# Performance work log

Measured on AMD Instinct MI355X. Metric: run time of the kernel, lower is better.

Reference implementation:

```python
import jax, jax.numpy as jnp
import numpy as np

B, C, H, W = 4, 3, 512, 960
K2 = 16  # 4x4 adaptive filter, DAIN-style


def setup_inputs() -> dict:
    key = jax.random.key(0)
    k1, k2, k3 = jax.random.split(key, 3)
    teninput = jax.random.normal(k1, (B, C, H, W), dtype=jnp.float32)
    tenflow = jax.random.normal(k2, (B, 2, H, W), dtype=jnp.float32)
    tenfilter = jax.random.uniform(k3, (B, K2, H, W), dtype=jnp.float32)
    return {"teninput": teninput, "tenflow": tenflow, "tenfilter": tenfilter}


def reference(teninput, tenflow, tenfilter):
    # DAIN FilterInterpolation forward:
    # out[b,c,y,x] = valid * sum_{dj,di < K} filter[b, dj*K+di, y, x]
    #               * bilinear(input, y2_T + dj + beta, x2_L + di + alpha)
    # with per-corner clamped gathers; out-of-bounds flow targets give 0.
    b, c, h, w = teninput.shape
    k2 = tenfilter.shape[1]
    K = int(np.sqrt(k2))

    dt = teninput.dtype
    xs = jnp.arange(w, dtype=dt)[None, None, :]
    ys = jnp.arange(h, dtype=dt)[None, :, None]
    fx, fy = tenflow[:, 0], tenflow[:, 1]          # [B,H,W]
    x2 = xs + fx
    y2 = ys + fy
    valid = ((x2 >= 0) & (x2 <= w - 1) & (y2 >= 0) & (y2 <= h - 1)
             & (jnp.abs(fx) < w / 2) & (jnp.abs(fy) < h / 2))

    ix = jnp.floor(x2).astype(jnp.int32)
    iy = jnp.floor(y2).astype(jnp.int32)
    alpha = (x2 - ix)[:, None]                     # [B,1,H,W]
    beta = (y2 - iy)[:, None]
    ixL0 = ix + 1 - K // 2                         # window left edge
    iyT0 = iy + 1 - K // 2                         # window top edge

    inp_flat = teninput.reshape(b, c, h * w)

    def gather(yi, xi):  # yi, xi: [B,H,W] int -> [B,C,H,W]
        idx = (yi * w + xi).reshape(b, 1, h * w)
        return jnp.take_along_axis(inp_flat, idx, axis=2).reshape(b, c, h, w)

    wTL = (1 - alpha) * (1 - beta)
    wTR = alpha * (1 - beta)
    wBL = (1 - alpha) * beta
    wBR = alpha * beta

    out = jnp.zeros_like(teninput)
    for dj in range(K):
        yT = jnp.clip(iyT0 + dj, 0, h - 1)
        yB = jnp.clip(iyT0 + dj + 1, 0, h - 1)
        for di in range(K):
            xL = jnp.clip(ixL0 + di, 0, w - 1)
            xR = jnp.clip(ixL0 + di + 1, 0, w - 1)
            val = (wTL * gather(yT, xL) + wTR * gather(yT, xR)
                   + wBL * gather(yB, xL) + wBR * gather(yB, xR))
            out = out + val * tenfilter[:, dj * K + di][:, None]

    return out * valid[:, None].astype(dt)
```

## Files before the change

### kernel.cpp

```cpp
#include <hip/hip_runtime.h>

#define BB 4
#define CC 3
#define HH 512
#define WW 960
#define HW (HH * WW)
#define NPIX (BB * HW)

__global__ __launch_bounds__(256)
void filter_interp_kernel(const float* __restrict__ inp,
                          const float* __restrict__ flow,
                          const float* __restrict__ filt,
                          float* __restrict__ out) {
    int tid = blockIdx.x * blockDim.x + threadIdx.x;
    if (tid >= NPIX) return;

    int b   = tid / HW;
    int rem = tid - b * HW;
    int y   = rem / WW;
    int x   = rem - y * WW;

    const float fx = flow[(b * 2 + 0) * HW + rem];
    const float fy = flow[(b * 2 + 1) * HW + rem];
    const float x2 = (float)x + fx;
    const float y2 = (float)y + fy;

    bool valid = (x2 >= 0.0f) && (x2 <= (float)(WW - 1)) &&
                 (y2 >= 0.0f) && (y2 <= (float)(HH - 1)) &&
                 (fabsf(fx) < (float)WW * 0.5f) &&
                 (fabsf(fy) < (float)HH * 0.5f);

    const int outbase = b * CC * HW + rem;
    if (!valid) {
        out[outbase]          = 0.0f;
        out[outbase + HW]     = 0.0f;
        out[outbase + 2 * HW] = 0.0f;
        return;
    }

    const int ix = (int)floorf(x2);
    const int iy = (int)floorf(y2);
    const float alpha = x2 - (float)ix;
    const float beta  = y2 - (float)iy;

    const float wTL = (1.0f - alpha) * (1.0f - beta);
    const float wTR = alpha * (1.0f - beta);
    const float wBL = (1.0f - alpha) * beta;
    const float wBR = alpha * beta;

    const int ixL0 = ix - 1;
    const int iyT0 = iy - 1;

    int R[5];
#pragma unroll
    for (int j = 0; j < 5; ++j) R[j] = min(max(iyT0 + j, 0), HH - 1);

    float Wm[5][5];
#pragma unroll
    for (int j = 0; j < 5; ++j)
#pragma unroll
        for (int i = 0; i < 5; ++i) Wm[j][i] = 0.0f;

    const float* fptr = filt + (size_t)b * 16 * HW + rem;
#pragma unroll
    for (int dj = 0; dj < 4; ++dj) {
#pragma unroll
        for (int di = 0; di < 4; ++di) {
            const float f = fptr[(size_t)(dj * 4 + di) * HW];
            Wm[dj][di]         += f * wTL;
            Wm[dj][di + 1]     += f * wTR;
            Wm[dj + 1][di]     += f * wBL;
            Wm[dj + 1][di + 1] += f * wBR;
        }
    }

    const float* ibase = inp + (size_t)b * CC * HW;
    float acc[3] = {0.0f, 0.0f, 0.0f};

    if (ixL0 >= 0 && ixL0 + 4 <= WW - 1) {
        const int a0 = ixL0 & ~3;
        const int o  = ixL0 - a0;

        const bool s2 = (o & 2) != 0;
        const bool s1 = (o & 1) != 0;
        float We[5][8];
#pragma unroll
        for (int j = 0; j < 5; ++j) {
            float t[8];
#pragma unroll
            for (int i = 0; i < 8; ++i) t[i] = (i < 5) ? Wm[j][i] : 0.0f;
            float u[8];
#pragma unroll
            for (int i = 0; i < 8; ++i)
                u[i] = s2 ? ((i >= 2) ? t[i - 2] : 0.0f) : t[i];
#pragma unroll
            for (int i = 0; i < 8; ++i)
                We[j][i] = s1 ? ((i >= 1) ? u[i - 1] : 0.0f) : u[i];
        }

#pragma unroll
        for (int j = 0; j < 5; ++j) {
            const size_t rowoff = (size_t)R[j] * WW + a0;
#pragma unroll
            for (int c = 0; c < CC; ++c) {
                const float* rp = ibase + (size_t)c * HW + rowoff;
                const float4 p0 = *(const float4*)(rp);
                const float4 p1 = *(const float4*)(rp + 4);
                float a = acc[c];
                a += p0.x * We[j][0];
                a += p0.y * We[j][1];
                a += p0.z * We[j][2];
                a += p0.w * We[j][3];
                a += p1.x * We[j][4];
                a += p1.y * We[j][5];
                a += p1.z * We[j][6];
                a += p1.w * We[j][7];
                acc[c] = a;
            }
        }
    } else {
        int S[5];
#pragma unroll
        for (int i = 0; i < 5; ++i) S[i] = min(max(ixL0 + i, 0), WW - 1);
#pragma unroll
        for (int c = 0; c < CC; ++c) {
            const float* ic = ibase + (size_t)c * HW;
            float a = 0.0f;
#pragma unroll
            for (int j = 0; j < 5; ++j) {
                const float* row = ic + (size_t)R[j] * WW;
#pragma unroll
                for (int i = 0; i < 5; ++i) a += row[S[i]] * Wm[j][i];
            }
            acc[c] = a;
        }
    }

    out[outbase]          = acc[0];
    out[outbase + HW]     = acc[1];
    out[outbase + 2 * HW] = acc[2];
}

extern "C" void kernel_launch(void* const* d_in, const int* in_sizes, int n_in,
                              void* d_out, int out_size, void* d_ws, size_t ws_size,
                              hipStream_t stream) {
    const float* teninput  = (const float*)d_in[0];
    const float* tenflow   = (const float*)d_in[1];
    const float* tenfilter = (const float*)d_in[2];
    float* out = (float*)d_out;

    const int threads = 256;
    const int blocks  = (NPIX + threads - 1) / threads;
    filter_interp_kernel<<<blocks, threads, 0, stream>>>(teninput, tenflow, tenfilter, out);
}
```

Before: 236.9 us.

## Stage input tile with halo in LDS for filter interpolation gathers

Each block now handles a 64x4 pixel tile and first cooperatively loads a 24x92 halo region of all three input channels into shared memory. Per-pixel 5x5 gathers are then served from shared memory when the flow target stays within the halo, with a global-memory fallback otherwise. This replaces scattered global gathers with shared reads, at the cost of a block-wide sync, redundant halo loading and higher LDS usage per block.

```diff
diff --git a/kernel.cpp b/kernel.cpp
--- a/kernel.cpp
+++ b/kernel.cpp
@@ -7,135 +7,171 @@
 #define HW (HH * WW)
 #define NPIX (BB * HW)
 
+#define TLX 64
+#define TLY 4
+#define NTX (WW / TLX)
+#define NTY (HH / TLY)
+#define NR 24
+#define RPAD 9
+#define NCOL 92
+#define CPAD 12
+
 __global__ __launch_bounds__(256)
-void filter_interp_kernel(const float* __restrict__ inp,
-                          const float* __restrict__ flow,
-                          const float* __restrict__ filt,
-                          float* __restrict__ out) {
-    int tid = blockIdx.x * blockDim.x + threadIdx.x;
-    if (tid >= NPIX) return;
+void filter_interp_tiled(const float* __restrict__ inp,
+                         const float* __restrict__ flow,
+                         const float* __restrict__ filt,
+                         float* __restrict__ out) {
+    const int lx = threadIdx.x & 63;
+    const int ly = threadIdx.x >> 6;
+    int blk = blockIdx.x;
+    const int tx = blk % NTX; blk /= NTX;
+    const int ty = blk % NTY;
+    const int b  = blk / NTY;
+    const int x0 = tx * TLX;
+    const int y0 = ty * TLY;
+    const int x  = x0 + lx;
+    const int y  = y0 + ly;
+    const int rem = y * WW + x;
 
-    int b   = tid / HW;
-    int rem = tid - b * HW;
-    int y   = rem / WW;
-    int x   = rem - y * WW;
+    __shared__ __align__(16) float sm[CC * NR * NCOL];
+
+    const float* ib = inp + (size_t)b * CC * HW;
+    const int c0 = x0 - CPAD;
+    const int r0 = y0 - RPAD;
+    for (int idx = threadIdx.x; idx < CC * NR * (NCOL / 4); idx += 256) {
+        const int ch = idx / (NR * (NCOL / 4));
+        const int rm = idx - ch * NR * (NCOL / 4);
+        const int r  = rm / (NCOL / 4);
+        const int m  = rm - r * (NCOL / 4);
+        const int gr = min(max(r0 + r, 0), HH - 1);
+        const int gcb = c0 + 4 * m;
+        const float* rowp = ib + (size_t)ch * HW + (size_t)gr * WW;
+        float4 v;
+        if (gcb >= 0 && gcb + 3 < WW) {
+            v = *(const float4*)(rowp + gcb);
+        } else {
+            v.x = rowp[min(max(gcb,     0), WW - 1)];
+            v.y = rowp[min(max(gcb + 1, 0), WW - 1)];
+            v.z = rowp[min(max(gcb + 2, 0), WW - 1)];
+            v.w = rowp[min(max(gcb + 3, 0), WW - 1)];
+        }
+        *(float4*)(&sm[(ch * NR + r) * NCOL + 4 * m]) = v;
+    }
+    __syncthreads();
 
     const float fx = flow[(b * 2 + 0) * HW + rem];
     const float fy = flow[(b * 2 + 1) * HW + rem];
     const float x2 = (float)x + fx;
     const float y2 = (float)y + fy;
 
-    bool valid = (x2 >= 0.0f) && (x2 <= (float)(WW - 1)) &&
-                 (y2 >= 0.0f) && (y2 <= (float)(HH - 1)) &&
-                 (fabsf(fx) < (float)WW * 0.5f) &&
-                 (fabsf(fy) < (float)HH * 0.5f);
+    const bool valid = (x2 >= 0.0f) && (x2 <= (float)(WW - 1)) &&
+                       (y2 >= 0.0f) && (y2 <= (float)(HH - 1)) &&
+                       (fabsf(fx) < (float)WW * 0.5f) &&
+                       (fabsf(fy) < (float)HH * 0.5f);
 
-    const int outbase = b * CC * HW + rem;
-    if (!valid) {
-        out[outbase]          = 0.0f;
-        out[outbase + HW]     = 0.0f;
-        out[outbase + 2 * HW] = 0.0f;
-        return;
-    }
+    float acc[3] = {0.0f, 0.0f, 0.0f};
 
-    const int ix = (int)floorf(x2);
-    const int iy = (int)floorf(y2);
-    const float alpha = x2 - (float)ix;
-    const float beta  = y2 - (float)iy;
+    if (valid) {
+        const int ix = (int)floorf(x2);
+        const int iy = (int)floorf(y2);
+        const float alpha = x2 - (float)ix;
+        const float beta  = y2 - (float)iy;
 
-    const float wTL = (1.0f - alpha) * (1.0f - beta);
-    const float wTR = alpha * (1.0f - beta);
-    const float wBL = (1.0f - alpha) * beta;
-    const float wBR = alpha * beta;
+        const float wTL = (1.0f - alpha) * (1.0f - beta);
+        const float wTR = alpha * (1.0f - beta);
+        const float wBL = (1.0f - alpha) * beta;
+        const float wBR = alpha * beta;
 
-    const int ixL0 = ix - 1;
-    const int iyT0 = iy - 1;
+        float Wm[5][5];
+#pragma unroll
+        for (int j = 0; j < 5; ++j)
+#pragma unroll
+            for (int i = 0; i < 5; ++i) Wm[j][i] = 0.0f;
 
-    int R[5];
+        const float* fptr = filt + (size_t)b * 16 * HW + rem;
 #pragma unroll
-    for (int j = 0; j < 5; ++j) R[j] = min(max(iyT0 + j, 0), HH - 1);
+        for (int dj = 0; dj < 4; ++dj) {
+#pragma unroll
+            for (int di = 0; di < 4; ++di) {
+                const float f = fptr[(size_t)(dj * 4 + di) * HW];
+                Wm[dj][di]         += f * wTL;
+                Wm[dj][di + 1]     += f * wTR;
+                Wm[dj + 1][di]     += f * wBL;
+                Wm[dj + 1][di + 1] += f * wBR;
+            }
+        }
 
-    float Wm[5][5];
+        const int ixL0 = ix - 1;
+        const int iyT0 = iy - 1;
+        const int k0 = iyT0 - r0;
+        const int d  = ixL0 - c0;
+        const int a0 = d & ~3;
+        const int o  = d & 3;
+
+        const bool fast = (k0 >= 0) && (k0 <= NR - 5) &&
+                          (d >= 0) && (a0 + 8 <= NCOL);
+
+        if (fast) {
+            const bool s2 = (o & 2) != 0;
+            const bool s1 = (o & 1) != 0;
+            float We[5][8];
 #pragma unroll
-    for (int j = 0; j < 5; ++j)
+            for (int j = 0; j < 5; ++j) {
+                float t[8];
 #pragma unroll
-        for (int i = 0; i < 5; ++i) Wm[j][i] = 0.0f;
+                for (int i = 0; i < 8; ++i) t[i] = (i < 5) ? Wm[j][i] : 0.0f;
+                float u[8];
+#pragma unroll
+                for (int i = 0; i < 8; ++i)
+                    u[i] = s2 ? ((i >= 2) ? t[i - 2] : 0.0f) : t[i];
+#pragma unroll
+                for (int i = 0; i < 8; ++i)
+                    We[j][i] = s1 ? ((i >= 1) ? u[i - 1] : 0.0f) : u[i];
+            }
 
-    const float* fptr = filt + (size_t)b * 16 * HW + rem;
 #pragma unroll
-    for (int dj = 0; dj < 4; ++dj) {
+            for (int j = 0; j < 5; ++j) {
+                const int rowbase = (k0 + j) * NCOL + a0;
 #pragma unroll
-        for (int di = 0; di < 4; ++di) {
-            const float f = fptr[(size_t)(dj * 4 + di) * HW];
-            Wm[dj][di]         += f * wTL;
-            Wm[dj][di + 1]     += f * wTR;
-            Wm[dj + 1][di]     += f * wBL;
-            Wm[dj + 1][di + 1] += f * wBR;
+                for (int c = 0; c < CC; ++c) {
+                    const float* sp = &sm[c * (NR * NCOL) + rowbase];
+                    const float4 p0 = *(const float4*)(sp);
+                    const float4 p1 = *(const float4*)(sp + 4);
+                    float a = acc[c];
+                    a += p0.x * We[j][0];
+                    a += p0.y * We[j][1];
+                    a += p0.z * We[j][2];
+                    a += p0.w * We[j][3];
+                    a += p1.x * We[j][4];
+                    a += p1.y * We[j][5];
+                    a += p1.z * We[j][6];
+                    a += p1.w * We[j][7];
+                    acc[c] = a;
+                }
+            }
+        } else {
+            int S[5], R[5];
+#pragma unroll
+            for (int i = 0; i < 5; ++i) {
+                S[i] = min(max(ixL0 + i, 0), WW - 1);
+                R[i] = min(max(iyT0 + i, 0), HH - 1);
+            }
+#pragma unroll
+            for (int c = 0; c < CC; ++c) {
+                const float* ic = ib + (size_t)c * HW;
+                float a = 0.0f;
+#pragma unroll
+                for (int j = 0; j < 5; ++j) {
+                    const float* row = ic + (size_t)R[j] * WW;
+#pragma unroll
+                    for (int i = 0; i < 5; ++i) a += row[S[i]] * Wm[j][i];
+                }
+                acc[c] = a;
+            }
         }
     }
 
-    const float* ibase = inp + (size_t)b * CC * HW;
-    float acc[3] = {0.0f, 0.0f, 0.0f};
-
-    if (ixL0 >= 0 && ixL0 + 4 <= WW - 1) {
-        const int a0 = ixL0 & ~3;
-        const int o  = ixL0 - a0;
-
-        const bool s2 = (o & 2) != 0;
-        const bool s1 = (o & 1) != 0;
-        float We[5][8];
-#pragma unroll
-        for (int j = 0; j < 5; ++j) {
-            float t[8];
-#pragma unroll
-            for (int i = 0; i < 8; ++i) t[i] = (i < 5) ? Wm[j][i] : 0.0f;
-            float u[8];
-#pragma unroll
-            for (int i = 0; i < 8; ++i)
-                u[i] = s2 ? ((i >= 2) ? t[i - 2] : 0.0f) : t[i];
-#pragma unroll
-            for (int i = 0; i < 8; ++i)
-                We[j][i] = s1 ? ((i >= 1) ? u[i - 1] : 0.0f) : u[i];
-        }
-
-#pragma unroll
-        for (int j = 0; j < 5; ++j) {
-            const size_t rowoff = (size_t)R[j] * WW + a0;
-#pragma unroll
-            for (int c = 0; c < CC; ++c) {
-                const float* rp = ibase + (size_t)c * HW + rowoff;
-                const float4 p0 = *(const float4*)(rp);
-                const float4 p1 = *(const float4*)(rp + 4);
-                float a = acc[c];
-                a += p0.x * We[j][0];
-                a += p0.y * We[j][1];
-                a += p0.z * We[j][2];
-                a += p0.w * We[j][3];
-                a += p1.x * We[j][4];
-                a += p1.y * We[j][5];
-                a += p1.z * We[j][6];
-                a += p1.w * We[j][7];
-                acc[c] = a;
-            }
-        }
-    } else {
-        int S[5];
-#pragma unroll
-        for (int i = 0; i < 5; ++i) S[i] = min(max(ixL0 + i, 0), WW - 1);
-#pragma unroll
-        for (int c = 0; c < CC; ++c) {
-            const float* ic = ibase + (size_t)c * HW;
-            float a = 0.0f;
-#pragma unroll
-            for (int j = 0; j < 5; ++j) {
-                const float* row = ic + (size_t)R[j] * WW;
-#pragma unroll
-                for (int i = 0; i < 5; ++i) a += row[S[i]] * Wm[j][i];
-            }
-            acc[c] = a;
-        }
-    }
-
+    const int outbase = b * CC * HW + rem;
     out[outbase]          = acc[0];
     out[outbase + HW]     = acc[1];
     out[outbase + 2 * HW] = acc[2];
@@ -149,7 +185,6 @@
     const float* tenfilter = (const float*)d_in[2];
     float* out = (float*)d_out;
 
-    const int threads = 256;
-    const int blocks  = (NPIX + threads - 1) / threads;
-    filter_interp_kernel<<<blocks, threads, 0, stream>>>(teninput, tenflow, tenfilter, out);
+    const int blocks = NTX * NTY * BB;
+    filter_interp_tiled<<<blocks, 256, 0, stream>>>(teninput, tenflow, tenfilter, out);
 }
```

New measurement: 255.9 us. 8.0% more time.

## Process four pixels per thread with vectorized flow, filter and output access

Applied to the files above, without the earlier changes.

Each thread now handles four horizontally adjacent pixels and loads flow, the 16 filter planes, and output stores as float4 vectors instead of scalar accesses. The gather work per pixel is unchanged and runs in a serial loop over the four pixels. This aims to cut memory instruction count and improve streaming efficiency on the dominant filter traffic. In exchange it raises register pressure (16 f4 filter values held live), lowers the thread count, and reduces latency hiding for the random gathers. Launch bounds now request 2 blocks per CU.

```diff
diff --git a/kernel.cpp b/kernel.cpp
--- a/kernel.cpp
+++ b/kernel.cpp
@@ -5,140 +5,156 @@
 #define HH 512
 #define WW 960
 #define HW (HH * WW)
-#define NPIX (BB * HW)
+#define NQ (BB * HW / 4)
 
-__global__ __launch_bounds__(256)
-void filter_interp_kernel(const float* __restrict__ inp,
-                          const float* __restrict__ flow,
-                          const float* __restrict__ filt,
-                          float* __restrict__ out) {
-    int tid = blockIdx.x * blockDim.x + threadIdx.x;
-    if (tid >= NPIX) return;
+typedef float f4 __attribute__((ext_vector_type(4)));
 
-    int b   = tid / HW;
-    int rem = tid - b * HW;
-    int y   = rem / WW;
-    int x   = rem - y * WW;
+__global__ __launch_bounds__(256, 2)
+void filter_interp_quad(const float* __restrict__ inp,
+                        const float* __restrict__ flow,
+                        const float* __restrict__ filt,
+                        float* __restrict__ out) {
+    const int t = blockIdx.x * 256 + threadIdx.x;
+    const int qpb = HW / 4;
+    const int b   = t / qpb;
+    const int q   = t - b * qpb;
+    const int y   = q / (WW / 4);
+    const int x0  = (q - y * (WW / 4)) * 4;
+    const int rem = y * WW + x0;
 
-    const float fx = flow[(b * 2 + 0) * HW + rem];
-    const float fy = flow[(b * 2 + 1) * HW + rem];
-    const float x2 = (float)x + fx;
-    const float y2 = (float)y + fy;
+    const f4 fx4 = *(const f4*)(flow + (size_t)(b * 2 + 0) * HW + rem);
+    const f4 fy4 = *(const f4*)(flow + (size_t)(b * 2 + 1) * HW + rem);
 
-    bool valid = (x2 >= 0.0f) && (x2 <= (float)(WW - 1)) &&
-                 (y2 >= 0.0f) && (y2 <= (float)(HH - 1)) &&
-                 (fabsf(fx) < (float)WW * 0.5f) &&
-                 (fabsf(fy) < (float)HH * 0.5f);
+    f4 ft[16];
+    const float* fb = filt + (size_t)b * 16 * HW + rem;
+#pragma unroll
+    for (int k = 0; k < 16; ++k) ft[k] = *(const f4*)(fb + (size_t)k * HW);
 
-    const int outbase = b * CC * HW + rem;
-    if (!valid) {
-        out[outbase]          = 0.0f;
-        out[outbase + HW]     = 0.0f;
-        out[outbase + 2 * HW] = 0.0f;
-        return;
+    const float* ib = inp + (size_t)b * CC * HW;
+
+    f4 accv[CC];
+#pragma unroll
+    for (int c = 0; c < CC; ++c) accv[c] = (f4){0.f, 0.f, 0.f, 0.f};
+
+#pragma unroll
+    for (int p = 0; p < 4; ++p) {
+        const float fx = fx4[p];
+        const float fy = fy4[p];
+        const int   xp = x0 + p;
+        const float x2 = (float)xp + fx;
+        const float y2 = (float)y + fy;
+
+        const bool valid = (x2 >= 0.0f) && (x2 <= (float)(WW - 1)) &&
+                           (y2 >= 0.0f) && (y2 <= (float)(HH - 1)) &&
+                           (fabsf(fx) < (float)WW * 0.5f) &&
+                           (fabsf(fy) < (float)HH * 0.5f);
+        if (!valid) continue;
+
+        const int ix = (int)floorf(x2);
+        const int iy = (int)floorf(y2);
+        const float alpha = x2 - (float)ix;
+        const float beta  = y2 - (float)iy;
+
+        const float wTL = (1.0f - alpha) * (1.0f - beta);
+        const float wTR = alpha * (1.0f - beta);
+        const float wBL = (1.0f - alpha) * beta;
+        const float wBR = alpha * beta;
+
+        float Wm[5][5];
+#pragma unroll
+        for (int j = 0; j < 5; ++j)
+#pragma unroll
+            for (int i = 0; i < 5; ++i) Wm[j][i] = 0.0f;
+#pragma unroll
+        for (int dj = 0; dj < 4; ++dj) {
+#pragma unroll
+            for (int di = 0; di < 4; ++di) {
+                const float f = ft[dj * 4 + di][p];
+                Wm[dj][di]         += f * wTL;
+                Wm[dj][di + 1]     += f * wTR;
+                Wm[dj + 1][di]     += f * wBL;
+                Wm[dj + 1][di + 1] += f * wBR;
+            }
+        }
+
+        const int ixL0 = ix - 1;
+        const int iyT0 = iy - 1;
+        int R[5];
+#pragma unroll
+        for (int j = 0; j < 5; ++j) R[j] = min(max(iyT0 + j, 0), HH - 1);
+
+        float a0c = 0.f, a1c = 0.f, a2c = 0.f;
+
+        if (ixL0 >= 0 && ixL0 + 4 <= WW - 1) {
+            const int a0 = ixL0 & ~3;
+            const int o  = ixL0 - a0;
+            const bool s2 = (o & 2) != 0;
+            const bool s1 = (o & 1) != 0;
+            float We[5][8];
+#pragma unroll
+            for (int j = 0; j < 5; ++j) {
+                float tt[8];
+#pragma unroll
+                for (int i = 0; i < 8; ++i) tt[i] = (i < 5) ? Wm[j][i] : 0.0f;
+                float u[8];
+#pragma unroll
+                for (int i = 0; i < 8; ++i)
+                    u[i] = s2 ? ((i >= 2) ? tt[i - 2] : 0.0f) : tt[i];
+#pragma unroll
+                for (int i = 0; i < 8; ++i)
+                    We[j][i] = s1 ? ((i >= 1) ? u[i - 1] : 0.0f) : u[i];
+            }
+
+#pragma unroll
+            for (int j = 0; j < 5; ++j) {
+                const size_t rowoff = (size_t)R[j] * WW + a0;
+                const float* r0p = ib + rowoff;
+                const float* r1p = r0p + HW;
+                const float* r2p = r1p + HW;
+                const f4 q00 = *(const f4*)(r0p);
+                const f4 q01 = *(const f4*)(r0p + 4);
+                const f4 q10 = *(const f4*)(r1p);
+                const f4 q11 = *(const f4*)(r1p + 4);
+                const f4 q20 = *(const f4*)(r2p);
+                const f4 q21 = *(const f4*)(r2p + 4);
+#pragma unroll
+                for (int i = 0; i < 4; ++i) {
+                    a0c += q00[i] * We[j][i];
+                    a0c += q01[i] * We[j][i + 4];
+                    a1c += q10[i] * We[j][i];
+                    a1c += q11[i] * We[j][i + 4];
+                    a2c += q20[i] * We[j][i];
+                    a2c += q21[i] * We[j][i + 4];
+                }
+            }
+        } else {
+            int S[5];
+#pragma unroll
+            for (int i = 0; i < 5; ++i) S[i] = min(max(ixL0 + i, 0), WW - 1);
+            float* accp[3] = {&a0c, &a1c, &a2c};
+#pragma unroll
+            for (int c = 0; c < CC; ++c) {
+                const float* ic = ib + (size_t)c * HW;
+                float a = 0.0f;
+#pragma unroll
+                for (int j = 0; j < 5; ++j) {
+                    const float* row = ic + (size_t)R[j] * WW;
+#pragma unroll
+                    for (int i = 0; i < 5; ++i) a += row[S[i]] * Wm[j][i];
+                }
+                *accp[c] = a;
+            }
+        }
+
+        accv[0][p] = a0c;
+        accv[1][p] = a1c;
+        accv[2][p] = a2c;
     }
 
-    const int ix = (int)floorf(x2);
-    const int iy = (int)floorf(y2);
-    const float alpha = x2 - (float)ix;
-    const float beta  = y2 - (float)iy;
-
-    const float wTL = (1.0f - alpha) * (1.0f - beta);
-    const float wTR = alpha * (1.0f - beta);
-    const float wBL = (1.0f - alpha) * beta;
-    const float wBR = alpha * beta;
-
-    const int ixL0 = ix - 1;
-    const int iyT0 = iy - 1;
-
-    int R[5];
-#pragma unroll
-    for (int j = 0; j < 5; ++j) R[j] = min(max(iyT0 + j, 0), HH - 1);
-
-    float Wm[5][5];
-#pragma unroll
-    for (int j = 0; j < 5; ++j)
-#pragma unroll
-        for (int i = 0; i < 5; ++i) Wm[j][i] = 0.0f;
-
-    const float* fptr = filt + (size_t)b * 16 * HW + rem;
-#pragma unroll
-    for (int dj = 0; dj < 4; ++dj) {
-#pragma unroll
-        for (int di = 0; di < 4; ++di) {
-            const float f = fptr[(size_t)(dj * 4 + di) * HW];
-            Wm[dj][di]         += f * wTL;
-            Wm[dj][di + 1]     += f * wTR;
-            Wm[dj + 1][di]     += f * wBL;
-            Wm[dj + 1][di + 1] += f * wBR;
-        }
-    }
-
-    const float* ibase = inp + (size_t)b * CC * HW;
-    float acc[3] = {0.0f, 0.0f, 0.0f};
-
-    if (ixL0 >= 0 && ixL0 + 4 <= WW - 1) {
-        const int a0 = ixL0 & ~3;
-        const int o  = ixL0 - a0;
-
-        const bool s2 = (o & 2) != 0;
-        const bool s1 = (o & 1) != 0;
-        float We[5][8];
-#pragma unroll
-        for (int j = 0; j < 5; ++j) {
-            float t[8];
-#pragma unroll
-            for (int i = 0; i < 8; ++i) t[i] = (i < 5) ? Wm[j][i] : 0.0f;
-            float u[8];
-#pragma unroll
-            for (int i = 0; i < 8; ++i)
-                u[i] = s2 ? ((i >= 2) ? t[i - 2] : 0.0f) : t[i];
-#pragma unroll
-            for (int i = 0; i < 8; ++i)
-                We[j][i] = s1 ? ((i >= 1) ? u[i - 1] : 0.0f) : u[i];
-        }
-
-#pragma unroll
-        for (int j = 0; j < 5; ++j) {
-            const size_t rowoff = (size_t)R[j] * WW + a0;
-#pragma unroll
-            for (int c = 0; c < CC; ++c) {
-                const float* rp = ibase + (size_t)c * HW + rowoff;
-                const float4 p0 = *(const float4*)(rp);
-                const float4 p1 = *(const float4*)(rp + 4);
-                float a = acc[c];
-                a += p0.x * We[j][0];
-                a += p0.y * We[j][1];
-                a += p0.z * We[j][2];
-                a += p0.w * We[j][3];
-                a += p1.x * We[j][4];
-                a += p1.y * We[j][5];
-                a += p1.z * We[j][6];
-                a += p1.w * We[j][7];
-                acc[c] = a;
-            }
-        }
-    } else {
-        int S[5];
-#pragma unroll
-        for (int i = 0; i < 5; ++i) S[i] = min(max(ixL0 + i, 0), WW - 1);
-#pragma unroll
-        for (int c = 0; c < CC; ++c) {
-            const float* ic = ibase + (size_t)c * HW;
-            float a = 0.0f;
-#pragma unroll
-            for (int j = 0; j < 5; ++j) {
-                const float* row = ic + (size_t)R[j] * WW;
-#pragma unroll
-                for (int i = 0; i < 5; ++i) a += row[S[i]] * Wm[j][i];
-            }
-            acc[c] = a;
-        }
-    }
-
-    out[outbase]          = acc[0];
-    out[outbase + HW]     = acc[1];
-    out[outbase + 2 * HW] = acc[2];
+    float* ob = out + (size_t)b * CC * HW + rem;
+    *(f4*)(ob)          = accv[0];
+    *(f4*)(ob + HW)     = accv[1];
+    *(f4*)(ob + 2 * HW) = accv[2];
 }
 
 extern "C" void kernel_launch(void* const* d_in, const int* in_sizes, int n_in,
@@ -149,7 +165,6 @@
     const float* tenfilter = (const float*)d_in[2];
     float* out = (float*)d_out;
 
-    const int threads = 256;
-    const int blocks  = (NPIX + threads - 1) / threads;
-    filter_interp_kernel<<<blocks, threads, 0, stream>>>(teninput, tenflow, tenfilter, out);
+    const int blocks = NQ / 256;
+    filter_interp_quad<<<blocks, 256, 0, stream>>>(teninput, tenflow, tenfilter, out);
 }
```

Measured after the change: 279.3 us. +17.9%, slower.

## Hoist filter and input-window loads, branchless invalid path, vector-accumulate taps

Applied to the files above, without the earlier changes.

All 16 filter taps are now loaded up front, along with all 30 float4 input-row loads for the fast path, so many memory requests are in flight before any arithmetic. Invalid pixels no longer return early. They are remapped to a safe in-bounds centre with zero weights, which keeps the wavefront from diverging but means those pixels now do the full gather. The 8-tap dot products are rewritten as float4 vector multiply-adds, and the indexing drops the tail bounds check. The cost is much higher register pressure (30 float4 plus 16 floats), which may reduce occupancy.

```diff
diff --git a/kernel.cpp b/kernel.cpp
--- a/kernel.cpp
+++ b/kernel.cpp
@@ -5,85 +5,99 @@
 #define HH 512
 #define WW 960
 #define HW (HH * WW)
-#define NPIX (BB * HW)
+
+typedef float f4 __attribute__((ext_vector_type(4)));
 
 __global__ __launch_bounds__(256)
-void filter_interp_kernel(const float* __restrict__ inp,
-                          const float* __restrict__ flow,
-                          const float* __restrict__ filt,
-                          float* __restrict__ out) {
-    int tid = blockIdx.x * blockDim.x + threadIdx.x;
-    if (tid >= NPIX) return;
+void filter_interp_batch(const float* __restrict__ inp,
+                         const float* __restrict__ flow,
+                         const float* __restrict__ filt,
+                         float* __restrict__ out) {
+    const int bpi = HW / 256;
+    const int b   = blockIdx.x / bpi;
+    const int rem = (blockIdx.x - b * bpi) * 256 + threadIdx.x;
+    const int y   = rem / WW;
+    const int x   = rem - y * WW;
 
-    int b   = tid / HW;
-    int rem = tid - b * HW;
-    int y   = rem / WW;
-    int x   = rem - y * WW;
+    const float* flb = flow + (size_t)(b * 2) * HW;
+    const float fx = flb[rem];
+    const float fy = flb[rem + HW];
 
-    const float fx = flow[(b * 2 + 0) * HW + rem];
-    const float fy = flow[(b * 2 + 1) * HW + rem];
+    float ftv[16];
+    const float* fb = filt + (size_t)(b * 16) * HW + rem;
+#pragma unroll
+    for (int k = 0; k < 16; ++k) ftv[k] = fb[(size_t)k * HW];
+
     const float x2 = (float)x + fx;
     const float y2 = (float)y + fy;
+    const bool valid = (x2 >= 0.0f) && (x2 <= (float)(WW - 1)) &&
+                       (y2 >= 0.0f) && (y2 <= (float)(HH - 1)) &&
+                       (fabsf(fx) < (float)WW * 0.5f) &&
+                       (fabsf(fy) < (float)HH * 0.5f);
 
-    bool valid = (x2 >= 0.0f) && (x2 <= (float)(WW - 1)) &&
-                 (y2 >= 0.0f) && (y2 <= (float)(HH - 1)) &&
-                 (fabsf(fx) < (float)WW * 0.5f) &&
-                 (fabsf(fy) < (float)HH * 0.5f);
+    const float fxf = floorf(x2);
+    const float fyf = floorf(y2);
+    const float alpha = valid ? (x2 - fxf) : 0.0f;
+    const float beta  = valid ? (y2 - fyf) : 0.0f;
+    const int   ix    = valid ? (int)fxf : 480;
+    const int   iy    = valid ? (int)fyf : 256;
+    const float vf    = valid ? 1.0f : 0.0f;
 
-    const int outbase = b * CC * HW + rem;
-    if (!valid) {
-        out[outbase]          = 0.0f;
-        out[outbase + HW]     = 0.0f;
-        out[outbase + 2 * HW] = 0.0f;
-        return;
-    }
-
-    const int ix = (int)floorf(x2);
-    const int iy = (int)floorf(y2);
-    const float alpha = x2 - (float)ix;
-    const float beta  = y2 - (float)iy;
-
-    const float wTL = (1.0f - alpha) * (1.0f - beta);
-    const float wTR = alpha * (1.0f - beta);
-    const float wBL = (1.0f - alpha) * beta;
-    const float wBR = alpha * beta;
+    const float wTL = vf * (1.0f - alpha) * (1.0f - beta);
+    const float wTR = vf * alpha * (1.0f - beta);
+    const float wBL = vf * (1.0f - alpha) * beta;
+    const float wBR = vf * alpha * beta;
 
     const int ixL0 = ix - 1;
     const int iyT0 = iy - 1;
-
     int R[5];
 #pragma unroll
     for (int j = 0; j < 5; ++j) R[j] = min(max(iyT0 + j, 0), HH - 1);
 
-    float Wm[5][5];
+    const float* ib = inp + (size_t)(b * CC) * HW;
+
+    f4 acc4[CC];
 #pragma unroll
-    for (int j = 0; j < 5; ++j)
-#pragma unroll
-        for (int i = 0; i < 5; ++i) Wm[j][i] = 0.0f;
+    for (int c = 0; c < CC; ++c) acc4[c] = (f4){0.f, 0.f, 0.f, 0.f};
+    float accs[CC] = {0.f, 0.f, 0.f};
 
-    const float* fptr = filt + (size_t)b * 16 * HW + rem;
-#pragma unroll
-    for (int dj = 0; dj < 4; ++dj) {
-#pragma unroll
-        for (int di = 0; di < 4; ++di) {
-            const float f = fptr[(size_t)(dj * 4 + di) * HW];
-            Wm[dj][di]         += f * wTL;
-            Wm[dj][di + 1]     += f * wTR;
-            Wm[dj + 1][di]     += f * wBL;
-            Wm[dj + 1][di + 1] += f * wBR;
-        }
-    }
-
-    const float* ibase = inp + (size_t)b * CC * HW;
-    float acc[3] = {0.0f, 0.0f, 0.0f};
-
-    if (ixL0 >= 0 && ixL0 + 4 <= WW - 1) {
+    const bool fast = (ixL0 >= 0) && (ixL0 <= WW - 5);
+    if (fast) {
         const int a0 = ixL0 & ~3;
         const int o  = ixL0 - a0;
 
+        f4 P[30];
+#pragma unroll
+        for (int j = 0; j < 5; ++j) {
+            const int ro = R[j] * WW + a0;
+#pragma unroll
+            for (int c = 0; c < CC; ++c) {
+                const float* p = ib + (size_t)c * HW + ro;
+                P[(j * 3 + c) * 2 + 0] = *(const f4*)(p);
+                P[(j * 3 + c) * 2 + 1] = *(const f4*)(p + 4);
+            }
+        }
+
+        float Wm[5][5];
+#pragma unroll
+        for (int j = 0; j < 5; ++j)
+#pragma unroll
+            for (int i = 0; i < 5; ++i) Wm[j][i] = 0.0f;
+#pragma unroll
+        for (int dj = 0; dj < 4; ++dj) {
+#pragma unroll
+            for (int di = 0; di < 4; ++di) {
+                const float f = ftv[dj * 4 + di];
+                Wm[dj][di]         += f * wTL;
+                Wm[dj][di + 1]     += f * wTR;
+                Wm[dj + 1][di]     += f * wBL;
+                Wm[dj + 1][di + 1] += f * wBR;
+            }
+        }
+
         const bool s2 = (o & 2) != 0;
         const bool s1 = (o & 1) != 0;
-        float We[5][8];
+        f4 WL[5], WH[5];
 #pragma unroll
         for (int j = 0; j < 5; ++j) {
             float t[8];
@@ -93,38 +107,45 @@
 #pragma unroll
             for (int i = 0; i < 8; ++i)
                 u[i] = s2 ? ((i >= 2) ? t[i - 2] : 0.0f) : t[i];
+            float w[8];
 #pragma unroll
             for (int i = 0; i < 8; ++i)
-                We[j][i] = s1 ? ((i >= 1) ? u[i - 1] : 0.0f) : u[i];
+                w[i] = s1 ? ((i >= 1) ? u[i - 1] : 0.0f) : u[i];
+            WL[j] = (f4){w[0], w[1], w[2], w[3]};
+            WH[j] = (f4){w[4], w[5], w[6], w[7]};
         }
 
 #pragma unroll
         for (int j = 0; j < 5; ++j) {
-            const size_t rowoff = (size_t)R[j] * WW + a0;
 #pragma unroll
             for (int c = 0; c < CC; ++c) {
-                const float* rp = ibase + (size_t)c * HW + rowoff;
-                const float4 p0 = *(const float4*)(rp);
-                const float4 p1 = *(const float4*)(rp + 4);
-                float a = acc[c];
-                a += p0.x * We[j][0];
-                a += p0.y * We[j][1];
-                a += p0.z * We[j][2];
-                a += p0.w * We[j][3];
-                a += p1.x * We[j][4];
-                a += p1.y * We[j][5];
-                a += p1.z * We[j][6];
-                a += p1.w * We[j][7];
-                acc[c] = a;
+                acc4[c] += P[(j * 3 + c) * 2 + 0] * WL[j];
+                acc4[c] += P[(j * 3 + c) * 2 + 1] * WH[j];
             }
         }
     } else {
+        float Wm[5][5];
+#pragma unroll
+        for (int j = 0; j < 5; ++j)
+#pragma unroll
+            for (int i = 0; i < 5; ++i) Wm[j][i] = 0.0f;
+#pragma unroll
+        for (int dj = 0; dj < 4; ++dj) {
+#pragma unroll
+            for (int di = 0; di < 4; ++di) {
+                const float f = ftv[dj * 4 + di];
+                Wm[dj][di]         += f * wTL;
+                Wm[dj][di + 1]     += f * wTR;
+                Wm[dj + 1][di]     += f * wBL;
+                Wm[dj + 1][di + 1] += f * wBR;
+            }
+        }
         int S[5];
 #pragma unroll
         for (int i = 0; i < 5; ++i) S[i] = min(max(ixL0 + i, 0), WW - 1);
 #pragma unroll
         for (int c = 0; c < CC; ++c) {
-            const float* ic = ibase + (size_t)c * HW;
+            const float* ic = ib + (size_t)c * HW;
             float a = 0.0f;
 #pragma unroll
             for (int j = 0; j < 5; ++j) {
@@ -132,13 +153,16 @@
 #pragma unroll
                 for (int i = 0; i < 5; ++i) a += row[S[i]] * Wm[j][i];
             }
-            acc[c] = a;
+            accs[c] = a;
         }
     }
 
-    out[outbase]          = acc[0];
-    out[outbase + HW]     = acc[1];
-    out[outbase + 2 * HW] = acc[2];
+    float* ob = out + (size_t)(b * CC) * HW + rem;
+#pragma unroll
+    for (int c = 0; c < CC; ++c) {
+        ob[(size_t)c * HW] =
+            acc4[c][0] + acc4[c][1] + acc4[c][2] + acc4[c][3] + accs[c];
+    }
 }
 
 extern "C" void kernel_launch(void* const* d_in, const int* in_sizes, int n_in,
@@ -149,7 +173,6 @@
     const float* tenfilter = (const float*)d_in[2];
     float* out = (float*)d_out;
 
-    const int threads = 256;
-    const int blocks  = (NPIX + threads - 1) / threads;
-    filter_interp_kernel<<<blocks, threads, 0, stream>>>(teninput, tenflow, tenfilter, out);
+    const int blocks = (BB * HW) / 256;
+    filter_interp_batch<<<blocks, 256, 0, stream>>>(teninput, tenflow, tenfilter, out);
 }
```

New measurement: 243.0 us. +2.6%, slower.
